# Optimization experiments

Measured on AMD Instinct MI355X. Metric: run time of the kernel, lower is better.

Reference implementation:

```python
import jax, jax.numpy as jnp
import numpy as np

B, H, S, D = 4, 16, 2048, 64
SCALING = 8.0  # sqrt(head_dim)

def setup_inputs() -> dict:
    key = jax.random.key(0)
    kq, kk, kv = jax.random.split(key, 3)
    q = jax.random.normal(kq, (B, H, S, D), dtype=jnp.float32)
    k = jax.random.normal(kk, (B, H, S, D), dtype=jnp.float32)
    v = jax.random.normal(kv, (B, H, S, D), dtype=jnp.float32)
    # causal mask, broadcastable [1,1,S,S]; mask==0 positions are masked out
    mask = jnp.tril(jnp.ones((S, S), dtype=jnp.int32))[None, None, :, :]
    return {"q": q, "k": k, "v": v, "mask": mask}

def reference(q, k, v, mask):
    # raw_attn = (q / scaling) @ k^T  -> [B,H,S,S]
    raw_attn = jnp.einsum("bhqd,bhkd->bhqk", q / SCALING, k)
    neg_inf = jnp.finfo(raw_attn.dtype).min
    raw_attn = jnp.where(mask == 0, neg_inf, raw_attn)
    attn = jax.nn.softmax(raw_attn, axis=-1)  # dropout p=0 in eval baseline
    output = jnp.einsum("bhqk,bhkd->bhqd", attn, v)
    return output, attn
```

## Files before the change

### kernel.cpp

```cpp
#include <hip/hip_runtime.h>
#include <cstdint>
#include <cstddef>


typedef __bf16 bf16x8 __attribute__((ext_vector_type(8)));
typedef float f32x4 __attribute__((ext_vector_type(4)));
typedef unsigned short us8 __attribute__((ext_vector_type(8)));
typedef unsigned short us4 __attribute__((ext_vector_type(4)));
typedef float fl4 __attribute__((ext_vector_type(4)));

#define QK_STR 72
#define P_STR 136

__device__ __forceinline__ unsigned short f2bf(float f) {
  unsigned int u = __builtin_bit_cast(unsigned int, f);
  u += 0x7FFFu + ((u >> 16) & 1u);
  return (unsigned short)(u >> 16);
}

__device__ __forceinline__ bf16x8 ld8(const unsigned short* p) {
  return __builtin_bit_cast(bf16x8, *(const us8*)p);
}

__global__ __launch_bounds__(256, 3) void attn_fwd(
    const float* __restrict__ Q, const float* __restrict__ K,
    const float* __restrict__ V, float* __restrict__ O,
    float* __restrict__ A) {
  __shared__ unsigned short ldsQK[18432];
  __shared__ unsigned short ldsV[64 * 136];

  unsigned short* const ldsQ = ldsQK;
  unsigned short* const ldsK = ldsQK + 9216;
  unsigned short* const ldsP = ldsQK;

  const int tid = threadIdx.x;
  const int bid = blockIdx.x;
  const int qt = 15 - (bid & 15);
  const int head = bid >> 4;
  const int q0 = qt * 128;

  const float* qg = Q + head * 131072 + q0 * 64;
  const float* kg = K + head * 131072;
  const float* vg = V + head * 131072;
  float* og = O + head * 131072 + q0 * 64;
  float* ag = A + (size_t)head * 4194304 + (size_t)q0 * 2048;

  const int wave = tid >> 6;
  const int lane = tid & 63;
  const int quad = lane >> 4;
  const int l15 = lane & 15;
  const int arow = wave * 32;

  {
    int w4 = (15 - qt) * 32;
    if (w4 > 0) {
      fl4 z = {0.f, 0.f, 0.f, 0.f};
      float* base = ag + (qt + 1) * 128;
      for (int r = tid >> 5; r < 128; r += 8) {
        float* rowp = base + (size_t)r * 2048;
        for (int c = tid & 31; c < w4; c += 32) *(fl4*)(rowp + c * 4) = z;
      }
    }
  }

  {
    int c4 = (tid & 15) * 4;
    int r0 = tid >> 4;
#pragma unroll
    for (int rp = 0; rp < 8; ++rp) {
      int row = rp * 16 + r0;
      fl4 x = *(const fl4*)(qg + row * 64 + c4);
      us4 o = {f2bf(x.x), f2bf(x.y), f2bf(x.z), f2bf(x.w)};
      *(us4*)(&ldsQ[row * QK_STR + c4]) = o;
    }
  }
  __syncthreads();

  bf16x8 qf[2][2];
#pragma unroll
  for (int mi = 0; mi < 2; ++mi)
#pragma unroll
    for (int ks = 0; ks < 2; ++ks)
      qf[mi][ks] = ld8(&ldsQ[(arow + mi * 16 + l15) * QK_STR + ks * 32 + quad * 8]);

  float lsum[2][4];
#pragma unroll
  for (int mi = 0; mi < 2; ++mi)
#pragma unroll
    for (int r = 0; r < 4; ++r) lsum[mi][r] = 0.f;

  for (int kt = 0; kt <= qt; ++kt) {
    __syncthreads();
    {
      int c4 = (tid & 15) * 4;
      int r0 = tid >> 4;
      const float* g = kg + kt * 8192;
#pragma unroll
      for (int rp = 0; rp < 8; ++rp) {
        int row = rp * 16 + r0;
        fl4 x = *(const fl4*)(g + row * 64 + c4);
        us4 o = {f2bf(x.x), f2bf(x.y), f2bf(x.z), f2bf(x.w)};
        *(us4*)(&ldsK[row * QK_STR + c4]) = o;
      }
    }
    __syncthreads();

    f32x4 sacc[2][8];
#pragma unroll
    for (int mi = 0; mi < 2; ++mi)
#pragma unroll
      for (int ni = 0; ni < 8; ++ni) sacc[mi][ni] = (f32x4){0.f, 0.f, 0.f, 0.f};
#pragma unroll
    for (int ni = 0; ni < 8; ++ni) {
      bf16x8 kf0 = ld8(&ldsK[(ni * 16 + l15) * QK_STR + quad * 8]);
      bf16x8 kf1 = ld8(&ldsK[(ni * 16 + l15) * QK_STR + 32 + quad * 8]);
#pragma unroll
      for (int mi = 0; mi < 2; ++mi) {
        sacc[mi][ni] = __builtin_amdgcn_mfma_f32_16x16x32_bf16(qf[mi][0], kf0, sacc[mi][ni], 0, 0, 0);
        sacc[mi][ni] = __builtin_amdgcn_mfma_f32_16x16x32_bf16(qf[mi][1], kf1, sacc[mi][ni], 0, 0, 0);
      }
    }
    const bool diag = (kt == qt);
#pragma unroll
    for (int mi = 0; mi < 2; ++mi)
#pragma unroll
      for (int ni = 0; ni < 8; ++ni) {
        int col_l = ni * 16 + l15;
#pragma unroll
        for (int r = 0; r < 4; ++r) {
          int row_l = arow + mi * 16 + quad * 4 + r;
          float p = __expf(sacc[mi][ni][r] * 0.125f);
          if (diag && col_l > row_l) p = 0.f;
          lsum[mi][r] += p;
        }
      }
  }

  float rinv[2][4];
#pragma unroll
  for (int mi = 0; mi < 2; ++mi)
#pragma unroll
    for (int r = 0; r < 4; ++r) {
      float t = lsum[mi][r];
      t += __shfl_xor(t, 1);
      t += __shfl_xor(t, 2);
      t += __shfl_xor(t, 4);
      t += __shfl_xor(t, 8);
      rinv[mi][r] = 1.0f / t;
    }

  f32x4 oacc[2][4];
#pragma unroll
  for (int mi = 0; mi < 2; ++mi)
#pragma unroll
    for (int nj = 0; nj < 4; ++nj) oacc[mi][nj] = (f32x4){0.f, 0.f, 0.f, 0.f};

  for (int kt = 0; kt <= qt; ++kt) {
    __syncthreads();
    {
      int c4 = (tid & 15) * 4;
      int r0 = tid >> 4;
      const float* g = kg + kt * 8192;
#pragma unroll
      for (int rp = 0; rp < 8; ++rp) {
        int row = rp * 16 + r0;
        fl4 x = *(const fl4*)(g + row * 64 + c4);
        us4 o = {f2bf(x.x), f2bf(x.y), f2bf(x.z), f2bf(x.w)};
        *(us4*)(&ldsK[row * QK_STR + c4]) = o;
      }
    }
    {
      int c4 = (tid & 15) * 4;
      int r0 = tid >> 4;
      const float* g = vg + kt * 8192;
#pragma unroll
      for (int rp = 0; rp < 8; ++rp) {
        int krow = rp * 16 + r0;
        fl4 x = *(const fl4*)(g + krow * 64 + c4);
        ldsV[(c4 + 0) * 136 + krow] = f2bf(x.x);
        ldsV[(c4 + 1) * 136 + krow] = f2bf(x.y);
        ldsV[(c4 + 2) * 136 + krow] = f2bf(x.z);
        ldsV[(c4 + 3) * 136 + krow] = f2bf(x.w);
      }
    }
    __syncthreads();

    f32x4 sacc[2][8];
#pragma unroll
    for (int mi = 0; mi < 2; ++mi)
#pragma unroll
      for (int ni = 0; ni < 8; ++ni) sacc[mi][ni] = (f32x4){0.f, 0.f, 0.f, 0.f};
#pragma unroll
    for (int ni = 0; ni < 8; ++ni) {
      bf16x8 kf0 = ld8(&ldsK[(ni * 16 + l15) * QK_STR + quad * 8]);
      bf16x8 kf1 = ld8(&ldsK[(ni * 16 + l15) * QK_STR + 32 + quad * 8]);
#pragma unroll
      for (int mi = 0; mi < 2; ++mi) {
        sacc[mi][ni] = __builtin_amdgcn_mfma_f32_16x16x32_bf16(qf[mi][0], kf0, sacc[mi][ni], 0, 0, 0);
        sacc[mi][ni] = __builtin_amdgcn_mfma_f32_16x16x32_bf16(qf[mi][1], kf1, sacc[mi][ni], 0, 0, 0);
      }
    }
    __syncthreads();
    const bool diag = (kt == qt);
#pragma unroll
    for (int mi = 0; mi < 2; ++mi)
#pragma unroll
      for (int ni = 0; ni < 8; ++ni) {
        int col_l = ni * 16 + l15;
#pragma unroll
        for (int r = 0; r < 4; ++r) {
          int row_l = arow + mi * 16 + quad * 4 + r;
          float p = __expf(sacc[mi][ni][r] * 0.125f);
          if (diag && col_l > row_l) p = 0.f;
          float a = p * rinv[mi][r];
          ag[(size_t)row_l * 2048 + kt * 128 + col_l] = a;
          ldsP[row_l * P_STR + col_l] = f2bf(a);
        }
      }
    __syncthreads();

#pragma unroll
    for (int ks = 0; ks < 4; ++ks) {
      bf16x8 pf0 = ld8(&ldsP[(arow + l15) * P_STR + ks * 32 + quad * 8]);
      bf16x8 pf1 = ld8(&ldsP[(arow + 16 + l15) * P_STR + ks * 32 + quad * 8]);
#pragma unroll
      for (int nj = 0; nj < 4; ++nj) {
        bf16x8 vf = ld8(&ldsV[(nj * 16 + l15) * 136 + ks * 32 + quad * 8]);
        oacc[0][nj] = __builtin_amdgcn_mfma_f32_16x16x32_bf16(pf0, vf, oacc[0][nj], 0, 0, 0);
        oacc[1][nj] = __builtin_amdgcn_mfma_f32_16x16x32_bf16(pf1, vf, oacc[1][nj], 0, 0, 0);
      }
    }
  }

#pragma unroll
  for (int mi = 0; mi < 2; ++mi)
#pragma unroll
    for (int nj = 0; nj < 4; ++nj)
#pragma unroll
      for (int r = 0; r < 4; ++r)
        og[(arow + mi * 16 + quad * 4 + r) * 64 + nj * 16 + l15] = oacc[mi][nj][r];
}

extern "C" void kernel_launch(void* const* d_in, const int* in_sizes, int n_in,
                              void* d_out, int out_size, void* d_ws, size_t ws_size,
                              hipStream_t stream) {
  const float* q = (const float*)d_in[0];
  const float* k = (const float*)d_in[1];
  const float* v = (const float*)d_in[2];
  float* out = (float*)d_out;
  float* attn = out + 8388608;
  hipLaunchKernelGGL(attn_fwd, dim3(1024), dim3(256), 0, stream, q, k, v, out, attn);
}
```

Measured before the change: 1.568 ms.

## Load K fragments directly from global memory, fold scaling into Q

K tiles are no longer staged through LDS. Each wave now reads its fp32 K fragments straight from global memory into registers and converts them to bf16 in place. This removes the LDS writes and the block barriers around K in both passes, plus the barrier between the P write and the P·V matmul, since each wave only reads back its own P rows. The 1/8 scale is folded into Q during conversion (exact, since it is a power of two), which drops a multiply per score. The cost is that all four waves redundantly fetch the full K tile through the cache, with 32-byte strided per-lane accesses.

```diff
diff --git a/kernel.cpp b/kernel.cpp
--- a/kernel.cpp
+++ b/kernel.cpp
@@ -11,6 +11,7 @@
 
 #define QK_STR 72
 #define P_STR 136
+#define V_STR 136
 
 __device__ __forceinline__ unsigned short f2bf(float f) {
   unsigned int u = __builtin_bit_cast(unsigned int, f);
@@ -22,16 +23,39 @@
   return __builtin_bit_cast(bf16x8, *(const us8*)p);
 }
 
+__device__ __forceinline__ bf16x8 cvt8(fl4 a, fl4 b) {
+  us8 o = {f2bf(a.x), f2bf(a.y), f2bf(a.z), f2bf(a.w),
+           f2bf(b.x), f2bf(b.y), f2bf(b.z), f2bf(b.w)};
+  return __builtin_bit_cast(bf16x8, o);
+}
+
+__device__ __forceinline__ void qk_tile(const float* krow_base,
+                                        const bf16x8 qf[2][2],
+                                        f32x4 sacc[2][8]) {
+#pragma unroll
+  for (int ni = 0; ni < 8; ++ni) {
+    const float* rp = krow_base + ni * 1024;
+    fl4 x0 = *(const fl4*)(rp);
+    fl4 x1 = *(const fl4*)(rp + 4);
+    fl4 y0 = *(const fl4*)(rp + 32);
+    fl4 y1 = *(const fl4*)(rp + 36);
+    bf16x8 kf0 = cvt8(x0, x1);
+    bf16x8 kf1 = cvt8(y0, y1);
+#pragma unroll
+    for (int mi = 0; mi < 2; ++mi) {
+      sacc[mi][ni] = __builtin_amdgcn_mfma_f32_16x16x32_bf16(qf[mi][0], kf0, sacc[mi][ni], 0, 0, 0);
+      sacc[mi][ni] = __builtin_amdgcn_mfma_f32_16x16x32_bf16(qf[mi][1], kf1, sacc[mi][ni], 0, 0, 0);
+    }
+  }
+}
+
 __global__ __launch_bounds__(256, 3) void attn_fwd(
     const float* __restrict__ Q, const float* __restrict__ K,
     const float* __restrict__ V, float* __restrict__ O,
     float* __restrict__ A) {
-  __shared__ unsigned short ldsQK[18432];
-  __shared__ unsigned short ldsV[64 * 136];
-
-  unsigned short* const ldsQ = ldsQK;
-  unsigned short* const ldsK = ldsQK + 9216;
-  unsigned short* const ldsP = ldsQK;
+  __shared__ unsigned short ldsP[128 * P_STR];
+  __shared__ unsigned short ldsV[64 * V_STR];
+  unsigned short* const ldsQ = ldsP;
 
   const int tid = threadIdx.x;
   const int bid = blockIdx.x;
@@ -70,7 +94,8 @@
     for (int rp = 0; rp < 8; ++rp) {
       int row = rp * 16 + r0;
       fl4 x = *(const fl4*)(qg + row * 64 + c4);
-      us4 o = {f2bf(x.x), f2bf(x.y), f2bf(x.z), f2bf(x.w)};
+      us4 o = {f2bf(x.x * 0.125f), f2bf(x.y * 0.125f),
+               f2bf(x.z * 0.125f), f2bf(x.w * 0.125f)};
       *(us4*)(&ldsQ[row * QK_STR + c4]) = o;
     }
   }
@@ -83,6 +108,8 @@
     for (int ks = 0; ks < 2; ++ks)
       qf[mi][ks] = ld8(&ldsQ[(arow + mi * 16 + l15) * QK_STR + ks * 32 + quad * 8]);
 
+  const float* kfrag_base = kg + l15 * 64 + quad * 8;
+
   float lsum[2][4];
 #pragma unroll
   for (int mi = 0; mi < 2; ++mi)
@@ -90,36 +117,13 @@
     for (int r = 0; r < 4; ++r) lsum[mi][r] = 0.f;
 
   for (int kt = 0; kt <= qt; ++kt) {
-    __syncthreads();
-    {
-      int c4 = (tid & 15) * 4;
-      int r0 = tid >> 4;
-      const float* g = kg + kt * 8192;
-#pragma unroll
-      for (int rp = 0; rp < 8; ++rp) {
-        int row = rp * 16 + r0;
-        fl4 x = *(const fl4*)(g + row * 64 + c4);
-        us4 o = {f2bf(x.x), f2bf(x.y), f2bf(x.z), f2bf(x.w)};
-        *(us4*)(&ldsK[row * QK_STR + c4]) = o;
-      }
-    }
-    __syncthreads();
-
     f32x4 sacc[2][8];
 #pragma unroll
     for (int mi = 0; mi < 2; ++mi)
 #pragma unroll
       for (int ni = 0; ni < 8; ++ni) sacc[mi][ni] = (f32x4){0.f, 0.f, 0.f, 0.f};
-#pragma unroll
-    for (int ni = 0; ni < 8; ++ni) {
-      bf16x8 kf0 = ld8(&ldsK[(ni * 16 + l15) * QK_STR + quad * 8]);
-      bf16x8 kf1 = ld8(&ldsK[(ni * 16 + l15) * QK_STR + 32 + quad * 8]);
-#pragma unroll
-      for (int mi = 0; mi < 2; ++mi) {
-        sacc[mi][ni] = __builtin_amdgcn_mfma_f32_16x16x32_bf16(qf[mi][0], kf0, sacc[mi][ni], 0, 0, 0);
-        sacc[mi][ni] = __builtin_amdgcn_mfma_f32_16x16x32_bf16(qf[mi][1], kf1, sacc[mi][ni], 0, 0, 0);
-      }
-    }
+    qk_tile(kfrag_base + kt * 8192, qf, sacc);
+
     const bool diag = (kt == qt);
 #pragma unroll
     for (int mi = 0; mi < 2; ++mi)
@@ -129,7 +133,7 @@
 #pragma unroll
         for (int r = 0; r < 4; ++r) {
           int row_l = arow + mi * 16 + quad * 4 + r;
-          float p = __expf(sacc[mi][ni][r] * 0.125f);
+          float p = __expf(sacc[mi][ni][r]);
           if (diag && col_l > row_l) p = 0.f;
           lsum[mi][r] += p;
         }
@@ -160,27 +164,15 @@
     {
       int c4 = (tid & 15) * 4;
       int r0 = tid >> 4;
-      const float* g = kg + kt * 8192;
-#pragma unroll
-      for (int rp = 0; rp < 8; ++rp) {
-        int row = rp * 16 + r0;
-        fl4 x = *(const fl4*)(g + row * 64 + c4);
-        us4 o = {f2bf(x.x), f2bf(x.y), f2bf(x.z), f2bf(x.w)};
-        *(us4*)(&ldsK[row * QK_STR + c4]) = o;
-      }
-    }
-    {
-      int c4 = (tid & 15) * 4;
-      int r0 = tid >> 4;
       const float* g = vg + kt * 8192;
 #pragma unroll
       for (int rp = 0; rp < 8; ++rp) {
         int krow = rp * 16 + r0;
         fl4 x = *(const fl4*)(g + krow * 64 + c4);
-        ldsV[(c4 + 0) * 136 + krow] = f2bf(x.x);
-        ldsV[(c4 + 1) * 136 + krow] = f2bf(x.y);
-        ldsV[(c4 + 2) * 136 + krow] = f2bf(x.z);
-        ldsV[(c4 + 3) * 136 + krow] = f2bf(x.w);
+        ldsV[(c4 + 0) * V_STR + krow] = f2bf(x.x);
+        ldsV[(c4 + 1) * V_STR + krow] = f2bf(x.y);
+        ldsV[(c4 + 2) * V_STR + krow] = f2bf(x.z);
+        ldsV[(c4 + 3) * V_STR + krow] = f2bf(x.w);
       }
     }
     __syncthreads();
@@ -190,17 +182,8 @@
     for (int mi = 0; mi < 2; ++mi)
 #pragma unroll
       for (int ni = 0; ni < 8; ++ni) sacc[mi][ni] = (f32x4){0.f, 0.f, 0.f, 0.f};
-#pragma unroll
-    for (int ni = 0; ni < 8; ++ni) {
-      bf16x8 kf0 = ld8(&ldsK[(ni * 16 + l15) * QK_STR + quad * 8]);
-      bf16x8 kf1 = ld8(&ldsK[(ni * 16 + l15) * QK_STR + 32 + quad * 8]);
-#pragma unroll
-      for (int mi = 0; mi < 2; ++mi) {
-        sacc[mi][ni] = __builtin_amdgcn_mfma_f32_16x16x32_bf16(qf[mi][0], kf0, sacc[mi][ni], 0, 0, 0);
-        sacc[mi][ni] = __builtin_amdgcn_mfma_f32_16x16x32_bf16(qf[mi][1], kf1, sacc[mi][ni], 0, 0, 0);
-      }
-    }
-    __syncthreads();
+    qk_tile(kfrag_base + kt * 8192, qf, sacc);
+
     const bool diag = (kt == qt);
 #pragma unroll
     for (int mi = 0; mi < 2; ++mi)
@@ -210,14 +193,13 @@
 #pragma unroll
         for (int r = 0; r < 4; ++r) {
           int row_l = arow + mi * 16 + quad * 4 + r;
-          float p = __expf(sacc[mi][ni][r] * 0.125f);
+          float p = __expf(sacc[mi][ni][r]);
           if (diag && col_l > row_l) p = 0.f;
           float a = p * rinv[mi][r];
           ag[(size_t)row_l * 2048 + kt * 128 + col_l] = a;
           ldsP[row_l * P_STR + col_l] = f2bf(a);
         }
       }
-    __syncthreads();
 
 #pragma unroll
     for (int ks = 0; ks < 4; ++ks) {
@@ -225,7 +207,7 @@
       bf16x8 pf1 = ld8(&ldsP[(arow + 16 + l15) * P_STR + ks * 32 + quad * 8]);
 #pragma unroll
       for (int nj = 0; nj < 4; ++nj) {
-        bf16x8 vf = ld8(&ldsV[(nj * 16 + l15) * 136 + ks * 32 + quad * 8]);
+        bf16x8 vf = ld8(&ldsV[(nj * 16 + l15) * V_STR + ks * 32 + quad * 8]);
         oacc[0][nj] = __builtin_amdgcn_mfma_f32_16x16x32_bf16(pf0, vf, oacc[0][nj], 0, 0, 0);
         oacc[1][nj] = __builtin_amdgcn_mfma_f32_16x16x32_bf16(pf1, vf, oacc[1][nj], 0, 0, 0);
       }
```

Measured after the change: 1.628 ms. 3.8% more time.
